# Kernel optimization log

Hardware: AMD Instinct MI355X
Metric: run time of the kernel (lower is better)

The kernel has to match this reference:

```python
import jax, jax.numpy as jnp
import numpy as np

T, B, H, L, A = 512, 128, 256, 2, 18


def setup_inputs() -> dict:
    key = jax.random.key(0)
    ks = jax.random.split(key, 10)
    s = 1.0 / np.sqrt(H)  # pytorch LSTM/Linear init scale
    return {
        "x": jax.random.normal(ks[0], (T, B, H), jnp.float32),
        "done": jax.random.bernoulli(ks[1], 0.05, (T, B)),
        "h0": jnp.zeros((L, B, H), jnp.float32),
        "c0": jnp.zeros((L, B, H), jnp.float32),
        "w_ih": jax.random.uniform(ks[2], (L, 4 * H, H), jnp.float32, -s, s),
        "w_hh": jax.random.uniform(ks[3], (L, 4 * H, H), jnp.float32, -s, s),
        "b_ih": jax.random.uniform(ks[4], (L, 4 * H), jnp.float32, -s, s),
        "b_hh": jax.random.uniform(ks[5], (L, 4 * H), jnp.float32, -s, s),
        "Wp": jax.random.uniform(ks[6], (A, H), jnp.float32, -s, s),
        "bp": jax.random.uniform(ks[7], (A,), jnp.float32, -s, s),
        "Wb": jax.random.uniform(ks[8], (1, H), jnp.float32, -s, s),
        "bb": jax.random.uniform(ks[9], (1,), jnp.float32, -s, s),
    }


def reference(x, done, h0, c0, w_ih, w_hh, b_ih, b_hh, Wp, bp, Wb, bb):
    def step(carry, inp):
        h, c = carry                      # [L,B,H] each
        xt, dt = inp                      # [B,H], [B]
        nd = (~dt).astype(xt.dtype)[None, :, None]  # reset state where done
        h = h * nd
        c = c * nd
        layer_in = xt
        hs, cs = [], []
        for l in range(L):
            gates = (layer_in @ w_ih[l].T + b_ih[l]
                     + h[l] @ w_hh[l].T + b_hh[l])      # [B,4H]
            i, f, g, o = jnp.split(gates, 4, axis=-1)   # pytorch gate order i,f,g,o
            i = jax.nn.sigmoid(i)
            f = jax.nn.sigmoid(f)
            g = jnp.tanh(g)
            o = jax.nn.sigmoid(o)
            cl = f * c[l] + i * g
            hl = o * jnp.tanh(cl)
            hs.append(hl)
            cs.append(cl)
            layer_in = hl
        return (jnp.stack(hs), jnp.stack(cs)), layer_in

    (hT, cT), core_out = jax.lax.scan(step, (h0, c0), (x, done))  # core_out: [T,B,H]
    flat = core_out.reshape(T * B, H)
    logits = flat @ Wp.T + bp                 # [T*B, A]
    baseline = (flat @ Wb.T + bb).reshape(T, B)
    action = jnp.argmax(logits, axis=1).reshape(T, B)  # eval-mode action
    policy_logits = logits.reshape(T, B, A)
    return policy_logits, baseline, action, hT, cT
```

## Files before the change

kernel.cpp:

```cpp
#include <hip/hip_runtime.h>
#include <math.h>

#define T_  512
#define B_  128
#define H_  256
#define A_  18
#define G4H 1024
#define TB_ (T_*B_)

#define OUT_BASE  (TB_*A_)
#define OUT_ACT   (OUT_BASE + TB_)
#define OUT_HT    (OUT_ACT + TB_)
#define OUT_CT    (OUT_HT + 2*B_*H_)

#define WS_H0  0
#define WS_H1  (2*B_*H_)
#define WS_C0  (4*B_*H_)
#define WS_C1  (5*B_*H_)
#define WS_CTR (6*B_*H_)


__device__ __forceinline__ float cload(const float* p) {
    return __hip_atomic_load((float*)p, __ATOMIC_RELAXED, __HIP_MEMORY_SCOPE_SYSTEM);
}
__device__ __forceinline__ float4 cload4(const float* p) {
    union { unsigned long long u[2]; float4 f; } r;
    r.u[0] = __hip_atomic_load((const unsigned long long*)p,
                               __ATOMIC_RELAXED, __HIP_MEMORY_SCOPE_SYSTEM);
    r.u[1] = __hip_atomic_load((const unsigned long long*)(p + 2),
                               __ATOMIC_RELAXED, __HIP_MEMORY_SCOPE_SYSTEM);
    return r.f;
}
__device__ __forceinline__ void cswap(float* p, float v) {
    float old = __hip_atomic_exchange(p, v, __ATOMIC_RELAXED, __HIP_MEMORY_SCOPE_SYSTEM);
    asm volatile("" :: "v"(old));
}

__global__ __launch_bounds__(512, 1) void lstm_persist(
    const float* __restrict__ x, const int* __restrict__ done,
    const float* __restrict__ h0in, const float* __restrict__ c0in,
    const float* __restrict__ w_ih, const float* __restrict__ w_hh,
    const float* __restrict__ b_ih, const float* __restrict__ b_hh,
    const float* __restrict__ Wp, const float* __restrict__ bp,
    const float* __restrict__ Wb, const float* __restrict__ bb,
    float* __restrict__ out, float* __restrict__ ws)
{
    __shared__ __align__(16) float wlds[64*2*H_];
    __shared__ __align__(16) float stg[16*H_];
    __shared__ __align__(16) float gates[4][16][17];
    __shared__ float hlog[19];

    const int wg   = blockIdx.x;
    const int tid  = threadIdx.x;
    const int l    = wg >> 7;
    const int wl   = wg & 127;
    const int lane = tid & 63;
    const int w    = tid >> 6;
    const int kc   = lane & 15;
    const int jq   = lane >> 4;
    const int bt   = wl >> 4, hg = wl & 15, b0 = bt*16;

    {
        const float* WI = w_ih + (size_t)l*G4H*H_;
        const float* WH = w_hh + (size_t)l*G4H*H_;
        float4* dst = (float4*)wlds;
        #pragma unroll
        for (int k = 0; k < 16; ++k) {
            const int idx = k*512 + tid;
            const int rs = idx >> 7, rem = idx & 127;
            const int m = rem >> 6, q4 = rem & 63;
            const int r = (rs >> 4)*256 + hg*16 + (rs & 15);
            const float* src = (m ? WH : WI) + (size_t)r*H_;
            dst[idx] = ((const float4*)src)[q4];
        }
    }

    float bsum[8];
    #pragma unroll
    for (int rr = 0; rr < 8; ++rr) {
        const int rs = w*8 + rr;
        const int r  = (rs >> 4)*256 + hg*16 + (rs & 15);
        bsum[rr] = b_ih[(size_t)l*G4H + r] + b_hh[(size_t)l*G4H + r];
    }
    float4 wpr[3]; float wpb[3];
    if (l == 1) {
        #pragma unroll
        for (int k = 0; k < 3; ++k) {
            const int a = w + 8*k;
            if (a < 19) {
                const float* wr = (a < 18) ? (Wp + (size_t)a*H_) : Wb;
                wpr[k] = ((const float4*)wr)[lane];
                wpb[k] = (a < 18) ? bp[a] : bb[0];
            }
        }
    }
    float cr = 0.f;

    const int sb = b0 + (tid >> 5);

    unsigned int* stamp = (unsigned int*)(ws + WS_CTR);
    __syncthreads();

    for (int p = 0; p < 514; ++p) {
        const int d = p;
        const int t = d - l;
        const bool work   = (t >= 0 && t < T_);
        const bool dohead = (l == 1 && d >= 2 && d - 2 < T_);

        if (dohead) {
            const int th = d - 2;
            const float* h1p = ws + WS_H1 + (size_t)(th & 1)*B_*H_ + (size_t)wl*H_ + lane*4;
            float4 h4 = cload4(h1p);
            #pragma unroll
            for (int k = 0; k < 3; ++k) {
                const int a = w + 8*k;
                if (a < 19) {
                    float s = wpr[k].x*h4.x + wpr[k].y*h4.y + wpr[k].z*h4.z + wpr[k].w*h4.w;
                    s += __shfl_xor(s, 1);  s += __shfl_xor(s, 2);  s += __shfl_xor(s, 4);
                    s += __shfl_xor(s, 8);  s += __shfl_xor(s, 16); s += __shfl_xor(s, 32);
                    if (lane == 0) {
                        float v = s + wpb[k];
                        hlog[a] = v;
                        if (a < 18) out[((size_t)th*B_ + wl)*A_ + a] = v;
                        else        out[OUT_BASE + th*B_ + wl] = v;
                    }
                }
            }
        }

        if (work) {
            float4 xr[4][4], hr[4][4];
            const float4* s4 = (const float4*)stg;

            if (l == 0) {
                const float4* xb0 = (const float4*)(x + ((size_t)t*B_ + b0)*H_);
                #pragma unroll
                for (int jj = 0; jj < 4; ++jj)
                    #pragma unroll
                    for (int q = 0; q < 4; ++q)
                        xr[jj][q] = xb0[(size_t)(jq*4 + jj)*64 + q*16 + kc];
            } else {
                const float* src = ws + WS_H0 + (size_t)(t&1)*B_*H_ + (size_t)b0*H_ + tid*8;
                float4 a = cload4(src), b2 = cload4(src + 4);
                ((float4*)stg)[tid*2]     = a;
                ((float4*)stg)[tid*2 + 1] = b2;
                __syncthreads();
                #pragma unroll
                for (int jj = 0; jj < 4; ++jj)
                    #pragma unroll
                    for (int q = 0; q < 4; ++q)
                        xr[jj][q] = s4[(jq*4 + jj)*64 + q*16 + kc];
                __syncthreads();
            }

            {
                const float nd = done[t*B_ + sb] ? 0.f : 1.f;
                float4 a, b2;
                if (t == 0) {
                    const float* src = h0in + (size_t)l*B_*H_ + (size_t)b0*H_ + tid*8;
                    a = ((const float4*)src)[0]; b2 = ((const float4*)src)[1];
                } else {
                    const float* src = ws + (l ? WS_H1 : WS_H0) + (size_t)((t-1)&1)*B_*H_
                                     + (size_t)b0*H_ + tid*8;
                    a = cload4(src); b2 = cload4(src + 4);
                }
                a.x *= nd;  a.y *= nd;  a.z *= nd;  a.w *= nd;
                b2.x *= nd; b2.y *= nd; b2.z *= nd; b2.w *= nd;
                ((float4*)stg)[tid*2]     = a;
                ((float4*)stg)[tid*2 + 1] = b2;
                __syncthreads();
                #pragma unroll
                for (int jj = 0; jj < 4; ++jj)
                    #pragma unroll
                    for (int q = 0; q < 4; ++q)
                        hr[jj][q] = s4[(jq*4 + jj)*64 + q*16 + kc];
            }

            const float4* wl4 = (const float4*)wlds;
            #pragma unroll 2
            for (int rr = 0; rr < 8; ++rr) {
                const int rs = w*8 + rr;
                const int g  = rs >> 4, ri = rs & 15;
                const int wb4 = rs*128;
                float4 wiv[4], whv[4];
                #pragma unroll
                for (int q = 0; q < 4; ++q) {
                    wiv[q] = wl4[wb4 + q*16 + kc];
                    whv[q] = wl4[wb4 + 64 + q*16 + kc];
                }
                float acc0 = 0.f, acc1 = 0.f, acc2 = 0.f, acc3 = 0.f;
                #pragma unroll
                for (int q = 0; q < 4; ++q) {
                    acc0 += wiv[q].x*xr[0][q].x + wiv[q].y*xr[0][q].y + wiv[q].z*xr[0][q].z + wiv[q].w*xr[0][q].w
                          + whv[q].x*hr[0][q].x + whv[q].y*hr[0][q].y + whv[q].z*hr[0][q].z + whv[q].w*hr[0][q].w;
                    acc1 += wiv[q].x*xr[1][q].x + wiv[q].y*xr[1][q].y + wiv[q].z*xr[1][q].z + wiv[q].w*xr[1][q].w
                          + whv[q].x*hr[1][q].x + whv[q].y*hr[1][q].y + whv[q].z*hr[1][q].z + whv[q].w*hr[1][q].w;
                    acc2 += wiv[q].x*xr[2][q].x + wiv[q].y*xr[2][q].y + wiv[q].z*xr[2][q].z + wiv[q].w*xr[2][q].w
                          + whv[q].x*hr[2][q].x + whv[q].y*hr[2][q].y + whv[q].z*hr[2][q].z + whv[q].w*hr[2][q].w;
                    acc3 += wiv[q].x*xr[3][q].x + wiv[q].y*xr[3][q].y + wiv[q].z*xr[3][q].z + wiv[q].w*xr[3][q].w
                          + whv[q].x*hr[3][q].x + whv[q].y*hr[3][q].y + whv[q].z*hr[3][q].z + whv[q].w*hr[3][q].w;
                }
                acc0 += __shfl_xor(acc0, 1, 16); acc0 += __shfl_xor(acc0, 2, 16);
                acc0 += __shfl_xor(acc0, 4, 16); acc0 += __shfl_xor(acc0, 8, 16);
                acc1 += __shfl_xor(acc1, 1, 16); acc1 += __shfl_xor(acc1, 2, 16);
                acc1 += __shfl_xor(acc1, 4, 16); acc1 += __shfl_xor(acc1, 8, 16);
                acc2 += __shfl_xor(acc2, 1, 16); acc2 += __shfl_xor(acc2, 2, 16);
                acc2 += __shfl_xor(acc2, 4, 16); acc2 += __shfl_xor(acc2, 8, 16);
                acc3 += __shfl_xor(acc3, 1, 16); acc3 += __shfl_xor(acc3, 2, 16);
                acc3 += __shfl_xor(acc3, 4, 16); acc3 += __shfl_xor(acc3, 8, 16);
                float v = (kc == 0) ? acc0 : (kc == 1) ? acc1 : (kc == 2) ? acc2 : acc3;
                if (kc < 4)
                    gates[g][ri][jq*4 + kc] = v + bsum[rr];
            }
        }

        __syncthreads();

        if (work && tid < 256) {
            const int j = tid >> 4, hi = tid & 15;
            const int b = b0 + j, h = hg*16 + hi;
            const float nd = done[t*B_ + b] ? 0.f : 1.f;
            if (t == 0) cr = c0in[(size_t)l*B_*H_ + b*H_ + h];
            float cp = cr * nd;
            const float gi = gates[0][hi][j], gf = gates[1][hi][j];
            const float gv = gates[2][hi][j], go = gates[3][hi][j];
            const float ii = 1.f/(1.f + expf(-gi));
            const float ff = 1.f/(1.f + expf(-gf));
            const float gt = tanhf(gv);
            const float oo = 1.f/(1.f + expf(-go));
            const float cl = ff*cp + ii*gt;
            cr = cl;
            if (t == T_-1)
                cswap(ws + (l ? WS_C1 : WS_C0) + (size_t)b*H_ + h, cl);
            float* hout = ws + (l ? WS_H1 : WS_H0) + (size_t)(t&1)*B_*H_;
            cswap(hout + (size_t)b*H_ + h, oo*tanhf(cl));
        }

        if (dohead && tid == 0) {
            const int th = d - 2;
            float best = hlog[0]; int bi = 0;
            #pragma unroll
            for (int a = 1; a < A_; ++a) { float v = hlog[a]; if (v > best) { best = v; bi = a; } }
            out[OUT_ACT + th*B_ + wl] = (float)bi;
        }

        if (l == 1 && d == 513 && tid < 256) {
            const int idx = wl*H_ + tid;
            out[OUT_HT + idx]         = cload(ws + WS_H0 + B_*H_ + idx);
            out[OUT_HT + B_*H_ + idx] = cload(ws + WS_H1 + B_*H_ + idx);
            out[OUT_CT + idx]         = cload(ws + WS_C0 + idx);
            out[OUT_CT + B_*H_ + idx] = cload(ws + WS_C1 + idx);
        }

        if (p < 513) {
            asm volatile("s_waitcnt vmcnt(0)" ::: "memory");
            __syncthreads();
            if (tid == 0)
                __hip_atomic_store(stamp + wg, (unsigned)(p + 1),
                                   __ATOMIC_RELAXED, __HIP_MEMORY_SCOPE_SYSTEM);
            if (tid < 32) {
                const int cell = (tid < 16) ? (bt*16 + tid) : (128 + bt*16 + (tid - 16));
                while (__hip_atomic_load(stamp + cell, __ATOMIC_RELAXED,
                                         __HIP_MEMORY_SCOPE_SYSTEM) <= (unsigned)p)
                    __builtin_amdgcn_s_sleep(1);
            }
            __syncthreads();
        }
    }
}

extern "C" void kernel_launch(void* const* d_in, const int* in_sizes, int n_in,
                              void* d_out, int out_size, void* d_ws, size_t ws_size,
                              hipStream_t stream)
{
    const float* x    = (const float*)d_in[0];
    const int*   done = (const int*)  d_in[1];
    const float* h0   = (const float*)d_in[2];
    const float* c0   = (const float*)d_in[3];
    const float* w_ih = (const float*)d_in[4];
    const float* w_hh = (const float*)d_in[5];
    const float* b_ih = (const float*)d_in[6];
    const float* b_hh = (const float*)d_in[7];
    const float* Wp   = (const float*)d_in[8];
    const float* bp   = (const float*)d_in[9];
    const float* Wb   = (const float*)d_in[10];
    const float* bb   = (const float*)d_in[11];
    float* out = (float*)d_out;
    float* ws  = (float*)d_ws;

    hipMemsetAsync((char*)d_ws + (size_t)WS_CTR*sizeof(float), 0, 1024, stream);

    lstm_persist<<<dim3(256), dim3(512), 0, stream>>>(
        x, done, h0, c0, w_ih, w_hh, b_ih, b_hh, Wp, bp, Wb, bb, out, ws);
}
```

Baseline: 6.542 ms.

## Keep gate values in registers, use DPP row reductions, move head to layer 0

Reorders the weight rows so each wave computes all four gates for the same hidden units. The gate activations can then run directly from registers, which removes the shared gates buffer and one block barrier per step. The 16-lane shuffle reductions are replaced with DPP row rotations. Global loads of h/x are issued at the top of the step so their latency overlaps the head. The policy/baseline head moves from layer-1 to layer-0 workgroups to balance the critical path. It adds register pressure from the full unroll and changes which threads own the cell state.

After: 7.345 ms. 1.12x slower.

```diff
diff --git a/kernel.cpp b/kernel.cpp
--- a/kernel.cpp
+++ b/kernel.cpp
@@ -34,6 +34,15 @@
 __device__ __forceinline__ void cswap(float* p, float v) {
     float old = __hip_atomic_exchange(p, v, __ATOMIC_RELAXED, __HIP_MEMORY_SCOPE_SYSTEM);
     asm volatile("" :: "v"(old));
+}
+template<int N>
+__device__ __forceinline__ float ror16(float v) {
+    return __int_as_float(__builtin_amdgcn_update_dpp(
+        0, __float_as_int(v), 0x120 | N, 0xF, 0xF, true));
+}
+__device__ __forceinline__ float rowsum16(float v) {
+    v += ror16<8>(v); v += ror16<4>(v); v += ror16<2>(v); v += ror16<1>(v);
+    return v;
 }
 
 __global__ __launch_bounds__(512, 1) void lstm_persist(
@@ -47,7 +56,6 @@
 {
     __shared__ __align__(16) float wlds[64*2*H_];
     __shared__ __align__(16) float stg[16*H_];
-    __shared__ __align__(16) float gates[4][16][17];
     __shared__ float hlog[19];
 
     const int wg   = blockIdx.x;
@@ -69,7 +77,7 @@
             const int idx = k*512 + tid;
             const int rs = idx >> 7, rem = idx & 127;
             const int m = rem >> 6, q4 = rem & 63;
-            const int r = (rs >> 4)*256 + hg*16 + (rs & 15);
+            const int r = ((rs & 7) >> 1)*256 + hg*16 + 2*(rs >> 3) + (rs & 1);
             const float* src = (m ? WH : WI) + (size_t)r*H_;
             dst[idx] = ((const float4*)src)[q4];
         }
@@ -78,12 +86,11 @@
     float bsum[8];
     #pragma unroll
     for (int rr = 0; rr < 8; ++rr) {
-        const int rs = w*8 + rr;
-        const int r  = (rs >> 4)*256 + hg*16 + (rs & 15);
+        const int r = (rr >> 1)*256 + hg*16 + 2*w + (rr & 1);
         bsum[rr] = b_ih[(size_t)l*G4H + r] + b_hh[(size_t)l*G4H + r];
     }
     float4 wpr[3]; float wpb[3];
-    if (l == 1) {
+    if (l == 0) {
         #pragma unroll
         for (int k = 0; k < 3; ++k) {
             const int a = w + 8*k;
@@ -95,27 +102,42 @@
         }
     }
     float cr = 0.f;
-
     const int sb = b0 + (tid >> 5);
 
     unsigned int* stamp = (unsigned int*)(ws + WS_CTR);
     __syncthreads();
 
     for (int p = 0; p < 514; ++p) {
-        const int d = p;
-        const int t = d - l;
+        const int t = p - l;
         const bool work   = (t >= 0 && t < T_);
-        const bool dohead = (l == 1 && d >= 2 && d - 2 < T_);
+        const bool dohead = (l == 0 && p >= 2);
+
+        float4 hh4;
+        if (dohead)
+            hh4 = cload4(ws + WS_H1 + (size_t)((p-2) & 1)*B_*H_ + (size_t)wl*H_ + lane*4);
+        float4 ha, hb, xa, xb;
+        if (work) {
+            if (t == 0) {
+                const float* src = h0in + (size_t)l*B_*H_ + (size_t)b0*H_ + tid*8;
+                ha = ((const float4*)src)[0]; hb = ((const float4*)src)[1];
+            } else {
+                const float* src = ws + (l ? WS_H1 : WS_H0) + (size_t)((t-1)&1)*B_*H_
+                                 + (size_t)b0*H_ + tid*8;
+                ha = cload4(src); hb = cload4(src + 4);
+            }
+            if (l == 1) {
+                const float* sx = ws + WS_H0 + (size_t)(t&1)*B_*H_ + (size_t)b0*H_ + tid*8;
+                xa = cload4(sx); xb = cload4(sx + 4);
+            }
+        }
 
         if (dohead) {
-            const int th = d - 2;
-            const float* h1p = ws + WS_H1 + (size_t)(th & 1)*B_*H_ + (size_t)wl*H_ + lane*4;
-            float4 h4 = cload4(h1p);
+            const int th = p - 2;
             #pragma unroll
             for (int k = 0; k < 3; ++k) {
                 const int a = w + 8*k;
                 if (a < 19) {
-                    float s = wpr[k].x*h4.x + wpr[k].y*h4.y + wpr[k].z*h4.z + wpr[k].w*h4.w;
+                    float s = wpr[k].x*hh4.x + wpr[k].y*hh4.y + wpr[k].z*hh4.z + wpr[k].w*hh4.w;
                     s += __shfl_xor(s, 1);  s += __shfl_xor(s, 2);  s += __shfl_xor(s, 4);
                     s += __shfl_xor(s, 8);  s += __shfl_xor(s, 16); s += __shfl_xor(s, 32);
                     if (lane == 0) {
@@ -128,22 +150,15 @@
             }
         }
 
+        float4 xr[4][4], hr[4][4];
+        const float4* s4 = (const float4*)stg;
         if (work) {
-            float4 xr[4][4], hr[4][4];
-            const float4* s4 = (const float4*)stg;
-
-            if (l == 0) {
-                const float4* xb0 = (const float4*)(x + ((size_t)t*B_ + b0)*H_);
-                #pragma unroll
-                for (int jj = 0; jj < 4; ++jj)
-                    #pragma unroll
-                    for (int q = 0; q < 4; ++q)
-                        xr[jj][q] = xb0[(size_t)(jq*4 + jj)*64 + q*16 + kc];
-            } else {
-                const float* src = ws + WS_H0 + (size_t)(t&1)*B_*H_ + (size_t)b0*H_ + tid*8;
-                float4 a = cload4(src), b2 = cload4(src + 4);
-                ((float4*)stg)[tid*2]     = a;
-                ((float4*)stg)[tid*2 + 1] = b2;
+            const float nd = done[t*B_ + sb] ? 0.f : 1.f;
+            ha.x *= nd; ha.y *= nd; ha.z *= nd; ha.w *= nd;
+            hb.x *= nd; hb.y *= nd; hb.z *= nd; hb.w *= nd;
+            if (l == 1) {
+                ((float4*)stg)[tid*2]     = xa;
+                ((float4*)stg)[tid*2 + 1] = xb;
                 __syncthreads();
                 #pragma unroll
                 for (int jj = 0; jj < 4; ++jj)
@@ -151,37 +166,42 @@
                     for (int q = 0; q < 4; ++q)
                         xr[jj][q] = s4[(jq*4 + jj)*64 + q*16 + kc];
                 __syncthreads();
-            }
-
-            {
-                const float nd = done[t*B_ + sb] ? 0.f : 1.f;
-                float4 a, b2;
-                if (t == 0) {
-                    const float* src = h0in + (size_t)l*B_*H_ + (size_t)b0*H_ + tid*8;
-                    a = ((const float4*)src)[0]; b2 = ((const float4*)src)[1];
-                } else {
-                    const float* src = ws + (l ? WS_H1 : WS_H0) + (size_t)((t-1)&1)*B_*H_
-                                     + (size_t)b0*H_ + tid*8;
-                    a = cload4(src); b2 = cload4(src + 4);
-                }
-                a.x *= nd;  a.y *= nd;  a.z *= nd;  a.w *= nd;
-                b2.x *= nd; b2.y *= nd; b2.z *= nd; b2.w *= nd;
-                ((float4*)stg)[tid*2]     = a;
-                ((float4*)stg)[tid*2 + 1] = b2;
-                __syncthreads();
+            } else {
+                const float4* xb0 = (const float4*)(x + ((size_t)t*B_ + b0)*H_);
                 #pragma unroll
                 for (int jj = 0; jj < 4; ++jj)
                     #pragma unroll
                     for (int q = 0; q < 4; ++q)
-                        hr[jj][q] = s4[(jq*4 + jj)*64 + q*16 + kc];
-            }
-
+                        xr[jj][q] = xb0[(size_t)(jq*4 + jj)*64 + q*16 + kc];
+            }
+            ((float4*)stg)[tid*2]     = ha;
+            ((float4*)stg)[tid*2 + 1] = hb;
+            __syncthreads();
+            #pragma unroll
+            for (int jj = 0; jj < 4; ++jj)
+                #pragma unroll
+                for (int q = 0; q < 4; ++q)
+                    hr[jj][q] = s4[(jq*4 + jj)*64 + q*16 + kc];
+        } else if (dohead) {
+            __syncthreads();
+        }
+
+        if (dohead && tid == 0) {
+            const int th = p - 2;
+            float best = hlog[0]; int bi = 0;
+            #pragma unroll
+            for (int a = 1; a < A_; ++a) { float v = hlog[a]; if (v > best) { best = v; bi = a; } }
+            out[OUT_ACT + th*B_ + wl] = (float)bi;
+        }
+
+        float myg[4];
+        if (work) {
             const float4* wl4 = (const float4*)wlds;
-            #pragma unroll 2
+            const int kb = kc & 3;
+            const int hs = kc >> 2;
+            #pragma unroll
             for (int rr = 0; rr < 8; ++rr) {
-                const int rs = w*8 + rr;
-                const int g  = rs >> 4, ri = rs & 15;
-                const int wb4 = rs*128;
+                const int wb4 = (w*8 + rr)*128;
                 float4 wiv[4], whv[4];
                 #pragma unroll
                 for (int q = 0; q < 4; ++q) {
@@ -200,34 +220,25 @@
                     acc3 += wiv[q].x*xr[3][q].x + wiv[q].y*xr[3][q].y + wiv[q].z*xr[3][q].z + wiv[q].w*xr[3][q].w
                           + whv[q].x*hr[3][q].x + whv[q].y*hr[3][q].y + whv[q].z*hr[3][q].z + whv[q].w*hr[3][q].w;
                 }
-                acc0 += __shfl_xor(acc0, 1, 16); acc0 += __shfl_xor(acc0, 2, 16);
-                acc0 += __shfl_xor(acc0, 4, 16); acc0 += __shfl_xor(acc0, 8, 16);
-                acc1 += __shfl_xor(acc1, 1, 16); acc1 += __shfl_xor(acc1, 2, 16);
-                acc1 += __shfl_xor(acc1, 4, 16); acc1 += __shfl_xor(acc1, 8, 16);
-                acc2 += __shfl_xor(acc2, 1, 16); acc2 += __shfl_xor(acc2, 2, 16);
-                acc2 += __shfl_xor(acc2, 4, 16); acc2 += __shfl_xor(acc2, 8, 16);
-                acc3 += __shfl_xor(acc3, 1, 16); acc3 += __shfl_xor(acc3, 2, 16);
-                acc3 += __shfl_xor(acc3, 4, 16); acc3 += __shfl_xor(acc3, 8, 16);
-                float v = (kc == 0) ? acc0 : (kc == 1) ? acc1 : (kc == 2) ? acc2 : acc3;
-                if (kc < 4)
-                    gates[g][ri][jq*4 + kc] = v + bsum[rr];
-            }
-        }
-
-        __syncthreads();
-
-        if (work && tid < 256) {
-            const int j = tid >> 4, hi = tid & 15;
-            const int b = b0 + j, h = hg*16 + hi;
+                acc0 = rowsum16(acc0); acc1 = rowsum16(acc1);
+                acc2 = rowsum16(acc2); acc3 = rowsum16(acc3);
+                const float gsel = (kb == 0) ? acc0 : (kb == 1) ? acc1
+                                 : (kb == 2) ? acc2 : acc3;
+                if (hs == (rr & 1))
+                    myg[rr >> 1] = gsel + bsum[rr];
+            }
+        }
+
+        if (work && kc < 8) {
+            const int b = b0 + jq*4 + (kc & 3);
+            const int h = hg*16 + 2*w + (kc >> 2);
             const float nd = done[t*B_ + b] ? 0.f : 1.f;
             if (t == 0) cr = c0in[(size_t)l*B_*H_ + b*H_ + h];
-            float cp = cr * nd;
-            const float gi = gates[0][hi][j], gf = gates[1][hi][j];
-            const float gv = gates[2][hi][j], go = gates[3][hi][j];
-            const float ii = 1.f/(1.f + expf(-gi));
-            const float ff = 1.f/(1.f + expf(-gf));
-            const float gt = tanhf(gv);
-            const float oo = 1.f/(1.f + expf(-go));
+            const float cp = cr * nd;
+            const float ii = 1.f/(1.f + expf(-myg[0]));
+            const float ff = 1.f/(1.f + expf(-myg[1]));
+            const float gt = tanhf(myg[2]);
+            const float oo = 1.f/(1.f + expf(-myg[3]));
             const float cl = ff*cp + ii*gt;
             cr = cl;
             if (t == T_-1)
@@ -236,15 +247,7 @@
             cswap(hout + (size_t)b*H_ + h, oo*tanhf(cl));
         }
 
-        if (dohead && tid == 0) {
-            const int th = d - 2;
-            float best = hlog[0]; int bi = 0;
-            #pragma unroll
-            for (int a = 1; a < A_; ++a) { float v = hlog[a]; if (v > best) { best = v; bi = a; } }
-            out[OUT_ACT + th*B_ + wl] = (float)bi;
-        }
-
-        if (l == 1 && d == 513 && tid < 256) {
+        if (l == 1 && p == 513 && tid < 256) {
             const int idx = wl*H_ + tid;
             out[OUT_HT + idx]         = cload(ws + WS_H0 + B_*H_ + idx);
             out[OUT_HT + B_*H_ + idx] = cload(ws + WS_H1 + B_*H_ + idx);
```
